# Performance work log

Measured on AMD Instinct MI355X. Metric: run time of the kernel, lower is better.

Reference implementation:

```python
import jax, jax.numpy as jnp
import numpy as np

B = 64          # batch
N = 256         # input_dim (number of MPS sites / pixels)
BOND = 128      # bond dimension
DF = 2          # feature dimension per pixel
OUT = 10        # output classes
EPS = 1e-12


def _xavier_uniform(key, shape, fan_in, fan_out, gain):
    bound = gain * np.sqrt(6.0 / (fan_in + fan_out))
    return jax.random.uniform(key, shape, jnp.float32, -bound, bound)


def setup_inputs() -> dict:
    key = jax.random.key(0)
    k_x, k_c0, k_cr, k_cl = jax.random.split(key, 4)
    gain = float(np.sqrt(2.0 / (1.0 + 0.01 ** 2)))  # leaky_relu gain
    x = jax.random.uniform(k_x, (B, N), dtype=jnp.float32)  # pixels in [0,1]
    # core 0: (1, DF, BOND); torch fan_in = DF*BOND, fan_out = 1*BOND
    core0 = _xavier_uniform(k_c0, (1, DF, BOND), DF * BOND, BOND, gain)
    # remaining N-1 cores: (BOND, DF, BOND); fan_in = DF*BOND, fan_out = BOND*BOND... torch: fan_in = shape[1]*shape[2] = DF*BOND, fan_out = shape[0]*shape[2] = BOND*BOND? No: fan_out = shape[0]*prod(shape[2:]) = BOND*BOND
    cores = _xavier_uniform(k_cr, (N - 1, BOND, DF, BOND), DF * BOND, BOND * BOND, gain)
    classifier = _xavier_uniform(k_cl, (OUT, BOND), BOND, OUT, gain)
    return {"x": x, "core0": core0, "cores": cores, "classifier": classifier}


def _mps_forward(x, core0, cores, classifier):
    b = x.shape[0]
    H = core0.shape[-1]
    # feature map: pixel v -> (1-v, v)
    feats = jnp.stack([1.0 - x, x], axis=-1)                  # (B, N, DF)
    # contract each core with its pixel feature
    special = jnp.einsum('ldh,bd->blh', core0, feats[:, 0])   # (B, 1, H)
    others = jnp.einsum('nldh,bnd->bnlh', cores, feats[:, 1:])  # (B, N-1, H, H)
    log_norm = jnp.zeros((b,), dtype=x.dtype)

    # log-depth tree contraction; loop bound is static (trace-time)
    while 1 + others.shape[1] > 1:
        # pad the special (1,H) leftmost tensor up to (H,H) with zero rows
        padded = jnp.pad(special, ((0, 0), (0, H - special.shape[1]), (0, 0)))
        full = jnp.concatenate([padded[:, None], others], axis=1)  # (B, K, H, H)
        K = full.shape[1]
        odd = (K % 2 != 0)
        if odd:
            last = full[:, -1]
            full = full[:, :-1]
        s1 = full[:, 0::2]                                    # (B, P, H, H)
        s2 = full[:, 1::2]
        cp = jnp.matmul(s1, s2)                               # (B, P, H, H)
        norms = jnp.maximum(
            jnp.sqrt(jnp.sum(cp * cp, axis=(-2, -1))), EPS)   # (B, P)
        log_norm = log_norm + jnp.sum(jnp.log(norms), axis=1)
        cp = cp / norms[:, :, None, None]
        special = cp[:, 0, 0:1, :]                            # keep only row 0
        others = cp[:, 1:]
        if odd:
            others = jnp.concatenate([others, last[:, None]], axis=1)

    mps_out = special[:, 0, :]                                # (B, H)
    logits = mps_out @ classifier.T + log_norm[:, None]      # (B, OUT)
    return logits


def reference(x, core0, cores, classifier):
    return _mps_forward(x, core0, cores, classifier)
```

## Files before the change

### kernel.cpp

```cpp
#include <hip/hip_runtime.h>
#include <stdint.h>


typedef unsigned short u16;
typedef __attribute__((ext_vector_type(8))) short short8;
typedef __attribute__((ext_vector_type(4))) float f32x4;

#define HP 136

__device__ __forceinline__ u16 f2b(float f) {
  uint32_t u = __builtin_bit_cast(uint32_t, f);
  u += 0x7FFFu + ((u >> 16) & 1u);
  return (u16)(u >> 16);
}
__device__ __forceinline__ float b2f(u16 b) {
  uint32_t u = ((uint32_t)b) << 16;
  return __builtin_bit_cast(float, u);
}

struct AccW { f32x4 t[2][2]; };

__device__ __forceinline__ void mfma_w16(const u16* Alds, const u16* Blds,
                                         AccW& acc) {
  const int tid = threadIdx.x;
  const int wid = tid >> 6, lane = tid & 63;
  const int wm = (wid >> 2) * 32, wn = (wid & 3) * 32;
  const int l16 = lane & 15, quad = lane >> 4;
#pragma unroll
  for (int tm = 0; tm < 2; tm++)
#pragma unroll
    for (int tn = 0; tn < 2; tn++)
      acc.t[tm][tn] = (f32x4){0.f, 0.f, 0.f, 0.f};
#pragma unroll
  for (int kk = 0; kk < 128; kk += 32) {
    short8 af[2], bf[2];
#pragma unroll
    for (int t = 0; t < 2; t++) {
      af[t] = *(const short8*)(Alds + (wm + t * 16 + l16) * HP + kk + quad * 8);
      bf[t] = *(const short8*)(Blds + (wn + t * 16 + l16) * HP + kk + quad * 8);
    }
#pragma unroll
    for (int tm = 0; tm < 2; tm++)
#pragma unroll
      for (int tn = 0; tn < 2; tn++)
        acc.t[tm][tn] = __builtin_amdgcn_mfma_f32_16x16x32_bf16(
            af[tm], bf[tn], acc.t[tm][tn], 0, 0, 0);
  }
}

__device__ __forceinline__ float acc_sumsq(const AccW& acc) {
  float ss = 0.f;
#pragma unroll
  for (int tm = 0; tm < 2; tm++)
#pragma unroll
    for (int tn = 0; tn < 2; tn++)
#pragma unroll
      for (int i = 0; i < 4; i++) {
        float v = acc.t[tm][tn][i];
        ss += v * v;
      }
  return ss;
}

__device__ __forceinline__ void bounce_store(u16* Lb, const AccW& acc, float scale,
                                             bool transposed) {
  const int tid = threadIdx.x;
  const int wid = tid >> 6, lane = tid & 63;
  const int wm = (wid >> 2) * 32, wn = (wid & 3) * 32;
  const int l16 = lane & 15, quad = lane >> 4;
#pragma unroll
  for (int tm = 0; tm < 2; tm++)
#pragma unroll
    for (int tn = 0; tn < 2; tn++)
#pragma unroll
      for (int i = 0; i < 4; i++) {
        int r = wm + tm * 16 + quad * 4 + i;
        int c = wn + tn * 16 + l16;
        int key = transposed ? c : r, sec = transposed ? r : c;
        Lb[key * HP + sec] = f2b(acc.t[tm][tn][i] * scale);
      }
}

__device__ __forceinline__ void copy_out(const u16* Lb, u16* out) {
  const int tid = threadIdx.x;
#pragma unroll
  for (int i = 0; i < 2; i++) {
    int g8 = tid + i * 1024;
    int row = g8 >> 4, c8 = g8 & 15;
    *(uint4*)(out + g8 * 8) = *(const uint4*)(Lb + row * HP + c8 * 8);
  }
}

__device__ __forceinline__ void loadM(u16* Lb, const u16* __restrict__ src) {
  const int tid = threadIdx.x;
#pragma unroll
  for (int i = 0; i < 2; i++) {
    int g8 = tid + i * 1024;
    int r = g8 >> 4, c8 = g8 & 15;
    *(uint4*)(Lb + r * HP + c8 * 8) = *(const uint4*)(src + g8 * 8);
  }
}

__device__ __forceinline__ float block_sum(float v, float* red, int nw) {
#pragma unroll
  for (int off = 32; off > 0; off >>= 1) v += __shfl_down(v, off);
  int wid = threadIdx.x >> 6;
  if ((threadIdx.x & 63) == 0) red[wid] = v;
  __syncthreads();
  if (threadIdx.x == 0) {
    float s = 0.f;
    for (int w = 0; w < nw; w++) s += red[w];
    red[0] = s;
  }
  __syncthreads();
  float s = red[0];
  __syncthreads();
  return s;
}

__device__ __forceinline__ float bsum16(float v, float* red) {
#pragma unroll
  for (int off = 32; off > 0; off >>= 1) v += __shfl_down(v, off);
  if ((threadIdx.x & 63) == 0) red[threadIdx.x >> 6] = v;
  __syncthreads();
  float s = 0.f;
#pragma unroll
  for (int w = 0; w < 16; w++) s += red[w];
  return s;
}

__global__ __launch_bounds__(1024) void k1(const float* __restrict__ cores,
                                           u16* __restrict__ T) {
  __shared__ u16 Ald[128 * HP], B0[128 * HP], B1[128 * HP];
  const int j = blockIdx.x;
  const int p = blockIdx.y;
  const float* c1 = cores + (size_t)(2 * j + 1) * 32768;
  const float* c2 = cores + (size_t)(2 * j + 2) * 32768;
  const int tid = threadIdx.x;
#pragma unroll 4
  for (int i = 0; i < 16; i++) {
    int lh = tid + i * 1024;
    int l = lh >> 7, h = lh & 127;
    float a0 = c1[(l * 2 + 0) * 128 + h];
    float av = p ? (c1[(l * 2 + 1) * 128 + h] - a0) : a0;
    Ald[l * HP + h] = f2b(av);
    float b0 = c2[(l * 2 + 0) * 128 + h];
    float b1 = c2[(l * 2 + 1) * 128 + h];
    B0[h * HP + l] = f2b(b0);
    B1[h * HP + l] = f2b(b1 - b0);
  }
  __syncthreads();
  const bool tr = (j % 2) == 0;
  u16* Tj = T + ((size_t)j * 4 + p * 2) * 16384;
  AccW q0, q1;
  mfma_w16(Ald, B0, q0);
  mfma_w16(Ald, B1, q1);
  __syncthreads();
  bounce_store(Ald, q0, 1.f, tr); __syncthreads();
  copy_out(Ald, Tj + 0 * 16384);  __syncthreads();
  bounce_store(Ald, q1, 1.f, tr); __syncthreads();
  copy_out(Ald, Tj + 1 * 16384);
}

__global__ __launch_bounds__(1024, 8) void k1b(const u16* __restrict__ T,
                                               u16* __restrict__ TT) {
  __shared__ u16 Ald[128 * HP], Bld[128 * HP];
  const int t = blockIdx.x;
  const int j2 = blockIdx.y;
  const int m1 = 2 * j2 + 1, m2 = 2 * j2 + 2;
  const u16* TA = T + ((size_t)m1 * 4 + (t >> 2)) * 16384;
  const u16* TB = T + ((size_t)m2 * 4 + (t & 3)) * 16384;
  loadM(Ald, TA);
  loadM(Bld, TB);
  __syncthreads();
  AccW acc;
  mfma_w16(Ald, Bld, acc);
  __syncthreads();
  bounce_store(Ald, acc, 1.f, (j2 % 2) == 0);
  __syncthreads();
  copy_out(Ald, TT + ((size_t)j2 * 16 + t) * 16384);
}

__global__ __launch_bounds__(256) void k1c(const u16* __restrict__ TT,
                                           float* __restrict__ Gpart) {
  __shared__ float Gp[1024];
  const int j2 = blockIdx.x, kc = blockIdx.y;
  const int tid = threadIdx.x;
  const int w = tid >> 6, lane = tid & 63;
  const int l16 = lane & 15, quad = lane >> 4;
  const u16* V = TT + (size_t)j2 * 16 * 16384 + (size_t)l16 * 16384;
  const int k0 = kc * 4096 + w * 1024;
  f32x4 acc = (f32x4){0.f, 0.f, 0.f, 0.f};
  for (int kk = k0; kk < k0 + 1024; kk += 32) {
    short8 av = *(const short8*)(V + kk + quad * 8);
    acc = __builtin_amdgcn_mfma_f32_16x16x32_bf16(av, av, acc, 0, 0, 0);
  }
#pragma unroll
  for (int i = 0; i < 4; i++)
    Gp[w * 256 + (quad * 4 + i) * 16 + l16] = acc[i];
  __syncthreads();
  Gpart[((size_t)j2 * 4 + kc) * 256 + tid] =
      Gp[tid] + Gp[256 + tid] + Gp[512 + tid] + Gp[768 + tid];
}

__global__ __launch_bounds__(128) void k2ns(const float* __restrict__ x,
                                            const float* __restrict__ Gpart,
                                            const float* __restrict__ core0,
                                            const float* __restrict__ cores,
                                            const u16* __restrict__ T,
                                            float* __restrict__ cbuf,
                                            float* __restrict__ sA,
                                            float* __restrict__ logs) {
  __shared__ float Gs[256];
  __shared__ float svec[128];
  __shared__ float red[8];
  const int bx = blockIdx.x, tid = threadIdx.x;
  if (bx < 63) {
    const int j2 = bx;
#pragma unroll
    for (int i = 0; i < 2; i++) {
      int t2 = tid + i * 128;
      float s = 0.f;
#pragma unroll
      for (int kc = 0; kc < 4; kc++)
        s += Gpart[((size_t)j2 * 4 + kc) * 256 + t2];
      Gs[t2] = s;
    }
    __syncthreads();
    if (tid < 64) {
      const int b = tid;
      const float* xb = x + b * 256;
      const int m1 = 2 * j2 + 1, m2 = 2 * j2 + 2;
      float a1 = xb[2 * m1 + 2], b1 = xb[2 * m1 + 3];
      float a2 = xb[2 * m2 + 2], b2 = xb[2 * m2 + 3];
      float c1[4] = {1.f, b1, a1, a1 * b1};
      float c2[4] = {1.f, b2, a2, a2 * b2};
      float c[16];
#pragma unroll
      for (int p = 0; p < 4; p++)
#pragma unroll
        for (int q = 0; q < 4; q++) c[p * 4 + q] = c1[p] * c2[q];
      float n2 = 0.f;
#pragma unroll
      for (int t = 0; t < 16; t++) {
        float s = 0.f;
#pragma unroll
        for (int u = 0; u < 16; u++) s += Gs[t * 16 + u] * c[u];
        n2 += c[t] * s;
      }
      float n = fmaxf(sqrtf(n2), 1e-12f);
      logs[b * 127 + 1 + j2] = logf(n);
      float inv = 1.f / n;
#pragma unroll
      for (int t = 0; t < 16; t++)
        cbuf[((size_t)j2 * 64 + b) * 16 + t] = c[t] * inv;
    }
  } else {
    const int b = bx - 63;
    const float* xb = x + b * 256;
    float x0 = xb[0], x1 = xb[1];
    svec[tid] = core0[tid] * (1.f - x0) + core0[128 + tid] * x0;
    __syncthreads();
    float acc1 = 0.f;
    for (int k = 0; k < 128; k++) {
      float m0 = cores[(k * 2 + 0) * 128 + tid];
      float m1 = cores[(k * 2 + 1) * 128 + tid];
      acc1 += svec[k] * (m0 + x1 * (m1 - m0));
    }
    float tot = block_sum(acc1 * acc1, red, 2);
    float n1 = fmaxf(sqrtf(tot), 1e-12f);
    float ln = logf(n1);
    svec[tid] = acc1 / n1;
    __syncthreads();
    float a = xb[2], bb = xb[3], ab = a * bb;
    float acc2 = 0.f;
    for (int k8 = 0; k8 < 16; k8++) {
      union { uint4 v; u16 s[8]; } q00, q01, q10, q11;
      q00.v = *(const uint4*)(T + tid * 128 + k8 * 8);
      q01.v = *(const uint4*)(T + 16384 + tid * 128 + k8 * 8);
      q10.v = *(const uint4*)(T + 32768 + tid * 128 + k8 * 8);
      q11.v = *(const uint4*)(T + 49152 + tid * 128 + k8 * 8);
#pragma unroll
      for (int e = 0; e < 8; e++) {
        float pk = b2f(q00.s[e]) + a * b2f(q10.s[e]) + bb * b2f(q01.s[e]) +
                   ab * b2f(q11.s[e]);
        acc2 += svec[k8 * 8 + e] * pk;
      }
    }
    float tot2 = block_sum(acc2 * acc2, red, 2);
    float n2 = fmaxf(sqrtf(tot2), 1e-12f);
    sA[b * 128 + tid] = acc2 / n2;
    if (tid == 0) logs[b * 127 + 0] = ln + logf(n2);
  }
}

__global__ __launch_bounds__(256, 4) void k2c(const u16* __restrict__ TT,
                                              const float* __restrict__ cbuf,
                                              u16* __restrict__ M0) {
  const int slice = blockIdx.x;
  const int j2 = blockIdx.y;
  const int tid = threadIdx.x;
  const int e0 = slice * 1024 + tid * 4;
  float v[16][4];
#pragma unroll
  for (int t = 0; t < 16; t++) {
    union { uint2 u; u16 s[4]; } q;
    q.u = *(const uint2*)(TT + ((size_t)j2 * 16 + t) * 16384 + e0);
#pragma unroll
    for (int e = 0; e < 4; e++) v[t][e] = b2f(q.s[e]);
  }
  const float4* cb4 = (const float4*)(cbuf + (size_t)j2 * 1024);
  u16* out = M0 + (size_t)j2 * 16384 + e0;
#pragma unroll 4
  for (int b = 0; b < 64; b++) {
    float4 c0 = cb4[b * 4 + 0];
    float4 c1 = cb4[b * 4 + 1];
    float4 c2 = cb4[b * 4 + 2];
    float4 c3 = cb4[b * 4 + 3];
    float cc[16] = {c0.x, c0.y, c0.z, c0.w, c1.x, c1.y, c1.z, c1.w,
                    c2.x, c2.y, c2.z, c2.w, c3.x, c3.y, c3.z, c3.w};
    float o[4] = {0.f, 0.f, 0.f, 0.f};
#pragma unroll
    for (int t = 0; t < 16; t++)
#pragma unroll
      for (int e = 0; e < 4; e++) o[e] += cc[t] * v[t][e];
    union { uint2 u; u16 s[4]; } r;
#pragma unroll
    for (int e = 0; e < 4; e++) r.s[e] = f2b(o[e]);
    *(uint2*)(out + (size_t)b * 63 * 16384) = r.u;
  }
}

__global__ __launch_bounds__(1024, 4) void round2x(const u16* __restrict__ In,
                                                   u16* __restrict__ Out,
                                                   const float* __restrict__ sIn,
                                                   float* __restrict__ sOut,
                                                   float* __restrict__ logs,
                                                   int count_in, int count_out,
                                                   int slot0, int slot1) {
  __shared__ u16 L0[128 * HP], L1[128 * HP];
  __shared__ float svf[256];
  __shared__ float red[16];
  const int b = blockIdx.y, p = blockIdx.x, tid = threadIdx.x;
  const u16* base = In + (size_t)b * count_in * 16384;
  if (p == 0) {
    if (tid < 128) svf[tid] = sIn[b * 128 + tid];
    loadM(L0, base + 1 * 16384);
    loadM(L1, base + 2 * 16384);
    __syncthreads();
    float acc0 = 0.f;
    if (tid < 128) {
      for (int k8 = 0; k8 < 16; k8++) {
        union { uint4 v; u16 s[8]; } q;
        q.v = *(const uint4*)(base + tid * 128 + k8 * 8);
#pragma unroll
        for (int e = 0; e < 8; e++) acc0 += svf[k8 * 8 + e] * b2f(q.s[e]);
      }
    }
    AccW accq;
    mfma_w16(L0, L1, accq);
    __syncthreads();
    bounce_store(L0, accq, 1.f, true);
    if (tid < 128) svf[128 + tid] = acc0;
    if (tid == 0) {
      logs[b * 127 + slot0] = 0.f;
      logs[b * 127 + slot0 + 1] = 0.f;
    }
    __syncthreads();
    float acc2 = 0.f;
    if (tid < 128) {
      for (int l = 0; l < 128; l++) acc2 += svf[128 + l] * b2f(L0[tid * HP + l]);
    }
    float t2 = bsum16((tid < 128) ? acc2 * acc2 : 0.f, red);
    float n2 = fmaxf(sqrtf(t2), 1e-12f);
    if (tid == 0) logs[b * 127 + slot1] = logf(n2);
    if (tid < 128) sOut[b * 128 + tid] = acc2 / n2;
  } else {
    const int m = p - 1;
    loadM(L0, base + (size_t)(4 * m + 3) * 16384);
    loadM(L1, base + (size_t)(4 * m + 4) * 16384);
    __syncthreads();
    AccW a1;
    mfma_w16(L0, L1, a1);
    __syncthreads();
    loadM(L0, base + (size_t)(4 * m + 5) * 16384);
    loadM(L1, base + (size_t)(4 * m + 6) * 16384);
    __syncthreads();
    AccW a2;
    mfma_w16(L0, L1, a2);
    __syncthreads();
    bounce_store(L0, a1, 1.f, false);
    bounce_store(L1, a2, 1.f, true);
    if (tid == 0) {
      logs[b * 127 + slot0 + 2 + 2 * m] = 0.f;
      logs[b * 127 + slot0 + 3 + 2 * m] = 0.f;
    }
    __syncthreads();
    AccW a3;
    mfma_w16(L0, L1, a3);
    float t3 = bsum16(acc_sumsq(a3), red);
    float n3 = fmaxf(sqrtf(t3), 1e-12f);
    if (tid == 0) logs[b * 127 + slot1 + 1 + m] = logf(n3);
    bounce_store(L0, a3, 1.f / n3, (m % 2) == 0);
    __syncthreads();
    copy_out(L0, Out + ((size_t)b * count_out + m) * 16384);
  }
}

__global__ __launch_bounds__(1024, 8) void r7f(const u16* __restrict__ In,
                                               const float* __restrict__ sIn,
                                               const float* __restrict__ logs,
                                               const float* __restrict__ cls,
                                               float* __restrict__ out) {
  __shared__ u16 Ald[128 * HP], Bld[128 * HP];
  __shared__ float svec[128], ovec[128], red[16];
  const int b = blockIdx.x, tid = threadIdx.x;
  if (tid < 128) svec[tid] = sIn[b * 128 + tid];
  loadM(Ald, In + ((size_t)b * 3 + 1) * 16384);
  loadM(Bld, In + ((size_t)b * 3 + 2) * 16384);
  __syncthreads();
  AccW acc;
  mfma_w16(Ald, Bld, acc);
  const u16* M0p = In + (size_t)b * 3 * 16384;
  float acc0 = 0.f;
  if (tid < 128) {
    for (int k8 = 0; k8 < 16; k8++) {
      union { uint4 v; u16 s[8]; } q;
      q.v = *(const uint4*)(M0p + tid * 128 + k8 * 8);
#pragma unroll
      for (int e = 0; e < 8; e++) acc0 += svec[k8 * 8 + e] * b2f(q.s[e]);
    }
  }
  __syncthreads();
  bounce_store(Ald, acc, 1.f, true);
  if (tid < 128) ovec[tid] = acc0;
  __syncthreads();
  float acc2 = 0.f;
  if (tid < 128) {
    for (int r = 0; r < 128; r++) acc2 += ovec[r] * b2f(Ald[tid * HP + r]);
  }
  float tot = bsum16((tid < 128) ? acc2 * acc2 : 0.f, red);
  float n = fmaxf(sqrtf(tot), 1e-12f);
  float lg = logf(n);
  if (tid < 128) svec[tid] = acc2 / n;
  __syncthreads();
  if (tid < 10) {
    float a = 0.f;
    for (int h = 0; h < 128; h++) a += svec[h] * cls[tid * 128 + h];
    float L = lg;
    for (int i = 0; i < 124; i++) L += logs[b * 127 + i];
    out[b * 10 + tid] = a + L;
  }
}

extern "C" void kernel_launch(void* const* d_in, const int* in_sizes, int n_in,
                              void* d_out, int out_size, void* d_ws, size_t ws_size,
                              hipStream_t stream) {
  (void)in_sizes; (void)n_in; (void)out_size; (void)ws_size;
  const float* x     = (const float*)d_in[0];
  const float* core0 = (const float*)d_in[1];
  const float* cores = (const float*)d_in[2];
  const float* cls   = (const float*)d_in[3];
  float* out = (float*)d_out;
  char* ws = (char*)d_ws;

  constexpr size_t SZ_T  = (size_t)127 * 4 * 16384 * 2;
  constexpr size_t SZ_A  = (size_t)64 * 31 * 16384 * 2;
  constexpr size_t SZ_M0 = (size_t)64 * 63 * 16384 * 2;

  u16*   T    = (u16*)(ws);
  u16*   TT   = (u16*)(ws + SZ_T);
  u16*   M2   = (u16*)(ws);
  u16*   M0   = (u16*)(ws + SZ_A);
  char*  tail0 = ws + SZ_A + SZ_M0;
  float* Gpart = (float*)(tail0);
  float* cbuf = (float*)(tail0 + 262144);
  float* sA   = (float*)(tail0 + 262144 + 262144);
  float* sB   = (float*)(tail0 + 262144 + 262144 + 32768);
  float* logs = (float*)(tail0 + 262144 + 262144 + 65536);

  k1  <<<dim3(127, 2), 1024, 0, stream>>>(cores, T);
  k1b <<<dim3(16, 63), 1024, 0, stream>>>(T, TT);
  k1c <<<dim3(63, 4), 256, 0, stream>>>(TT, Gpart);
  k2ns<<<dim3(127), 128, 0, stream>>>(x, Gpart, core0, cores, T, cbuf, sA, logs);
  k2c <<<dim3(16, 63), 256, 0, stream>>>(TT, cbuf, M0);
  round2x<<<dim3(16, 64), 1024, 0, stream>>>(M0, M2, sA, sB, logs, 63, 15, 64, 96);
  round2x<<<dim3(4, 64), 1024, 0, stream>>>(M2, M0, sB, sA, logs, 15, 3, 112, 120);
  r7f  <<<dim3(64), 1024, 0, stream>>>(M0, sA, logs, cls, out);
}
```

Measured before the change: 247.3 us.

## Replace precomputed 16-term pair products with per-batch fused matmul in k2f

```diff
diff --git a/kernel.cpp b/kernel.cpp
--- a/kernel.cpp
+++ b/kernel.cpp
@@ -162,173 +162,109 @@
   copy_out(Ald, Tj + 1 * 16384);
 }
 
-__global__ __launch_bounds__(1024, 8) void k1b(const u16* __restrict__ T,
-                                               u16* __restrict__ TT) {
-  __shared__ u16 Ald[128 * HP], Bld[128 * HP];
-  const int t = blockIdx.x;
-  const int j2 = blockIdx.y;
-  const int m1 = 2 * j2 + 1, m2 = 2 * j2 + 2;
-  const u16* TA = T + ((size_t)m1 * 4 + (t >> 2)) * 16384;
-  const u16* TB = T + ((size_t)m2 * 4 + (t & 3)) * 16384;
-  loadM(Ald, TA);
-  loadM(Bld, TB);
-  __syncthreads();
-  AccW acc;
-  mfma_w16(Ald, Bld, acc);
-  __syncthreads();
-  bounce_store(Ald, acc, 1.f, (j2 % 2) == 0);
-  __syncthreads();
-  copy_out(Ald, TT + ((size_t)j2 * 16 + t) * 16384);
-}
-
-__global__ __launch_bounds__(256) void k1c(const u16* __restrict__ TT,
-                                           float* __restrict__ Gpart) {
-  __shared__ float Gp[1024];
-  const int j2 = blockIdx.x, kc = blockIdx.y;
-  const int tid = threadIdx.x;
-  const int w = tid >> 6, lane = tid & 63;
-  const int l16 = lane & 15, quad = lane >> 4;
-  const u16* V = TT + (size_t)j2 * 16 * 16384 + (size_t)l16 * 16384;
-  const int k0 = kc * 4096 + w * 1024;
-  f32x4 acc = (f32x4){0.f, 0.f, 0.f, 0.f};
-  for (int kk = k0; kk < k0 + 1024; kk += 32) {
-    short8 av = *(const short8*)(V + kk + quad * 8);
-    acc = __builtin_amdgcn_mfma_f32_16x16x32_bf16(av, av, acc, 0, 0, 0);
-  }
-#pragma unroll
-  for (int i = 0; i < 4; i++)
-    Gp[w * 256 + (quad * 4 + i) * 16 + l16] = acc[i];
-  __syncthreads();
-  Gpart[((size_t)j2 * 4 + kc) * 256 + tid] =
-      Gp[tid] + Gp[256 + tid] + Gp[512 + tid] + Gp[768 + tid];
+__global__ __launch_bounds__(1024, 4) void k2f(const u16* __restrict__ T,
+                                               const float* __restrict__ x,
+                                               u16* __restrict__ M0,
+                                               float* __restrict__ logs) {
+  __shared__ u16 L0[128 * HP], L1[128 * HP];
+  __shared__ float red[16];
+  const int j2 = blockIdx.x, g = blockIdx.y, tid = threadIdx.x;
+  const u16* TA = T + ((size_t)(2 * j2 + 1) * 4) * 16384;
+  const u16* TB = T + ((size_t)(2 * j2 + 2) * 4) * 16384;
+  uint4 rA[2][4], rB[2][4];
+#pragma unroll
+  for (int i = 0; i < 2; i++) {
+    int gg = (tid + i * 1024) * 8;
+#pragma unroll
+    for (int p = 0; p < 4; p++) {
+      rA[i][p] = *(const uint4*)(TA + (size_t)p * 16384 + gg);
+      rB[i][p] = *(const uint4*)(TB + (size_t)p * 16384 + gg);
+    }
+  }
+  for (int bb = 0; bb < 8; bb++) {
+    const int b = g * 8 + bb;
+    const float* xb = x + b * 256;
+    float a1 = xb[4 * j2 + 4], b1 = xb[4 * j2 + 5];
+    float a2 = xb[4 * j2 + 6], b2 = xb[4 * j2 + 7];
+    float ab1 = a1 * b1, ab2 = a2 * b2;
+#pragma unroll
+    for (int i = 0; i < 2; i++) {
+      int gg = tid + i * 1024;
+      int row = gg >> 4, c8 = gg & 15;
+      union { uint4 v; u16 s[8]; } q0, q1, q2, q3, oA, oB;
+      q0.v = rA[i][0]; q1.v = rA[i][1]; q2.v = rA[i][2]; q3.v = rA[i][3];
+#pragma unroll
+      for (int e = 0; e < 8; e++) {
+        float v = b2f(q0.s[e]) + b1 * b2f(q1.s[e]) + a1 * b2f(q2.s[e]) +
+                  ab1 * b2f(q3.s[e]);
+        oA.s[e] = f2b(v);
+      }
+      q0.v = rB[i][0]; q1.v = rB[i][1]; q2.v = rB[i][2]; q3.v = rB[i][3];
+#pragma unroll
+      for (int e = 0; e < 8; e++) {
+        float v = b2f(q0.s[e]) + b2 * b2f(q1.s[e]) + a2 * b2f(q2.s[e]) +
+                  ab2 * b2f(q3.s[e]);
+        oB.s[e] = f2b(v);
+      }
+      *(uint4*)(L0 + row * HP + c8 * 8) = oA.v;
+      *(uint4*)(L1 + row * HP + c8 * 8) = oB.v;
+    }
+    __syncthreads();
+    AccW acc;
+    mfma_w16(L0, L1, acc);
+    float t = bsum16(acc_sumsq(acc), red);
+    float n = fmaxf(sqrtf(t), 1e-12f);
+    if (tid == 0) logs[b * 127 + 1 + j2] = logf(n);
+    bounce_store(L0, acc, 1.f / n, (j2 % 2) == 0);
+    __syncthreads();
+    copy_out(L0, M0 + ((size_t)b * 63 + j2) * 16384);
+    __syncthreads();
+  }
 }
 
 __global__ __launch_bounds__(128) void k2ns(const float* __restrict__ x,
-                                            const float* __restrict__ Gpart,
                                             const float* __restrict__ core0,
                                             const float* __restrict__ cores,
                                             const u16* __restrict__ T,
-                                            float* __restrict__ cbuf,
                                             float* __restrict__ sA,
                                             float* __restrict__ logs) {
-  __shared__ float Gs[256];
   __shared__ float svec[128];
   __shared__ float red[8];
-  const int bx = blockIdx.x, tid = threadIdx.x;
-  if (bx < 63) {
-    const int j2 = bx;
-#pragma unroll
-    for (int i = 0; i < 2; i++) {
-      int t2 = tid + i * 128;
-      float s = 0.f;
-#pragma unroll
-      for (int kc = 0; kc < 4; kc++)
-        s += Gpart[((size_t)j2 * 4 + kc) * 256 + t2];
-      Gs[t2] = s;
-    }
-    __syncthreads();
-    if (tid < 64) {
-      const int b = tid;
-      const float* xb = x + b * 256;
-      const int m1 = 2 * j2 + 1, m2 = 2 * j2 + 2;
-      float a1 = xb[2 * m1 + 2], b1 = xb[2 * m1 + 3];
-      float a2 = xb[2 * m2 + 2], b2 = xb[2 * m2 + 3];
-      float c1[4] = {1.f, b1, a1, a1 * b1};
-      float c2[4] = {1.f, b2, a2, a2 * b2};
-      float c[16];
-#pragma unroll
-      for (int p = 0; p < 4; p++)
-#pragma unroll
-        for (int q = 0; q < 4; q++) c[p * 4 + q] = c1[p] * c2[q];
-      float n2 = 0.f;
-#pragma unroll
-      for (int t = 0; t < 16; t++) {
-        float s = 0.f;
-#pragma unroll
-        for (int u = 0; u < 16; u++) s += Gs[t * 16 + u] * c[u];
-        n2 += c[t] * s;
-      }
-      float n = fmaxf(sqrtf(n2), 1e-12f);
-      logs[b * 127 + 1 + j2] = logf(n);
-      float inv = 1.f / n;
-#pragma unroll
-      for (int t = 0; t < 16; t++)
-        cbuf[((size_t)j2 * 64 + b) * 16 + t] = c[t] * inv;
-    }
-  } else {
-    const int b = bx - 63;
-    const float* xb = x + b * 256;
-    float x0 = xb[0], x1 = xb[1];
-    svec[tid] = core0[tid] * (1.f - x0) + core0[128 + tid] * x0;
-    __syncthreads();
-    float acc1 = 0.f;
-    for (int k = 0; k < 128; k++) {
-      float m0 = cores[(k * 2 + 0) * 128 + tid];
-      float m1 = cores[(k * 2 + 1) * 128 + tid];
-      acc1 += svec[k] * (m0 + x1 * (m1 - m0));
-    }
-    float tot = block_sum(acc1 * acc1, red, 2);
-    float n1 = fmaxf(sqrtf(tot), 1e-12f);
-    float ln = logf(n1);
-    svec[tid] = acc1 / n1;
-    __syncthreads();
-    float a = xb[2], bb = xb[3], ab = a * bb;
-    float acc2 = 0.f;
-    for (int k8 = 0; k8 < 16; k8++) {
-      union { uint4 v; u16 s[8]; } q00, q01, q10, q11;
-      q00.v = *(const uint4*)(T + tid * 128 + k8 * 8);
-      q01.v = *(const uint4*)(T + 16384 + tid * 128 + k8 * 8);
-      q10.v = *(const uint4*)(T + 32768 + tid * 128 + k8 * 8);
-      q11.v = *(const uint4*)(T + 49152 + tid * 128 + k8 * 8);
-#pragma unroll
-      for (int e = 0; e < 8; e++) {
-        float pk = b2f(q00.s[e]) + a * b2f(q10.s[e]) + bb * b2f(q01.s[e]) +
-                   ab * b2f(q11.s[e]);
-        acc2 += svec[k8 * 8 + e] * pk;
-      }
-    }
-    float tot2 = block_sum(acc2 * acc2, red, 2);
-    float n2 = fmaxf(sqrtf(tot2), 1e-12f);
-    sA[b * 128 + tid] = acc2 / n2;
-    if (tid == 0) logs[b * 127 + 0] = ln + logf(n2);
-  }
-}
-
-__global__ __launch_bounds__(256, 4) void k2c(const u16* __restrict__ TT,
-                                              const float* __restrict__ cbuf,
-                                              u16* __restrict__ M0) {
-  const int slice = blockIdx.x;
-  const int j2 = blockIdx.y;
-  const int tid = threadIdx.x;
-  const int e0 = slice * 1024 + tid * 4;
-  float v[16][4];
-#pragma unroll
-  for (int t = 0; t < 16; t++) {
-    union { uint2 u; u16 s[4]; } q;
-    q.u = *(const uint2*)(TT + ((size_t)j2 * 16 + t) * 16384 + e0);
-#pragma unroll
-    for (int e = 0; e < 4; e++) v[t][e] = b2f(q.s[e]);
-  }
-  const float4* cb4 = (const float4*)(cbuf + (size_t)j2 * 1024);
-  u16* out = M0 + (size_t)j2 * 16384 + e0;
-#pragma unroll 4
-  for (int b = 0; b < 64; b++) {
-    float4 c0 = cb4[b * 4 + 0];
-    float4 c1 = cb4[b * 4 + 1];
-    float4 c2 = cb4[b * 4 + 2];
-    float4 c3 = cb4[b * 4 + 3];
-    float cc[16] = {c0.x, c0.y, c0.z, c0.w, c1.x, c1.y, c1.z, c1.w,
-                    c2.x, c2.y, c2.z, c2.w, c3.x, c3.y, c3.z, c3.w};
-    float o[4] = {0.f, 0.f, 0.f, 0.f};
-#pragma unroll
-    for (int t = 0; t < 16; t++)
-#pragma unroll
-      for (int e = 0; e < 4; e++) o[e] += cc[t] * v[t][e];
-    union { uint2 u; u16 s[4]; } r;
-#pragma unroll
-    for (int e = 0; e < 4; e++) r.s[e] = f2b(o[e]);
-    *(uint2*)(out + (size_t)b * 63 * 16384) = r.u;
-  }
+  const int b = blockIdx.x, tid = threadIdx.x;
+  const float* xb = x + b * 256;
+  float x0 = xb[0], x1 = xb[1];
+  svec[tid] = core0[tid] * (1.f - x0) + core0[128 + tid] * x0;
+  __syncthreads();
+  float acc1 = 0.f;
+  for (int k = 0; k < 128; k++) {
+    float m0 = cores[(k * 2 + 0) * 128 + tid];
+    float m1 = cores[(k * 2 + 1) * 128 + tid];
+    acc1 += svec[k] * (m0 + x1 * (m1 - m0));
+  }
+  float tot = block_sum(acc1 * acc1, red, 2);
+  float n1 = fmaxf(sqrtf(tot), 1e-12f);
+  float ln = logf(n1);
+  svec[tid] = acc1 / n1;
+  __syncthreads();
+  float a = xb[2], bb = xb[3], ab = a * bb;
+  float acc2 = 0.f;
+  for (int k8 = 0; k8 < 16; k8++) {
+    union { uint4 v; u16 s[8]; } q00, q01, q10, q11;
+    q00.v = *(const uint4*)(T + tid * 128 + k8 * 8);
+    q01.v = *(const uint4*)(T + 16384 + tid * 128 + k8 * 8);
+    q10.v = *(const uint4*)(T + 32768 + tid * 128 + k8 * 8);
+    q11.v = *(const uint4*)(T + 49152 + tid * 128 + k8 * 8);
+#pragma unroll
+    for (int e = 0; e < 8; e++) {
+      float pk = b2f(q00.s[e]) + a * b2f(q10.s[e]) + bb * b2f(q01.s[e]) +
+                 ab * b2f(q11.s[e]);
+      acc2 += svec[k8 * 8 + e] * pk;
+    }
+  }
+  float tot2 = block_sum(acc2 * acc2, red, 2);
+  float n2 = fmaxf(sqrtf(tot2), 1e-12f);
+  sA[b * 128 + tid] = acc2 / n2;
+  if (tid == 0) logs[b * 127 + 0] = ln + logf(n2);
 }
 
 __global__ __launch_bounds__(1024, 4) void round2x(const u16* __restrict__ In,
@@ -464,26 +400,20 @@
   float* out = (float*)d_out;
   char* ws = (char*)d_ws;
 
-  constexpr size_t SZ_T  = (size_t)127 * 4 * 16384 * 2;
   constexpr size_t SZ_A  = (size_t)64 * 31 * 16384 * 2;
   constexpr size_t SZ_M0 = (size_t)64 * 63 * 16384 * 2;
 
   u16*   T    = (u16*)(ws);
-  u16*   TT   = (u16*)(ws + SZ_T);
   u16*   M2   = (u16*)(ws);
   u16*   M0   = (u16*)(ws + SZ_A);
   char*  tail0 = ws + SZ_A + SZ_M0;
-  float* Gpart = (float*)(tail0);
-  float* cbuf = (float*)(tail0 + 262144);
   float* sA   = (float*)(tail0 + 262144 + 262144);
   float* sB   = (float*)(tail0 + 262144 + 262144 + 32768);
   float* logs = (float*)(tail0 + 262144 + 262144 + 65536);
 
   k1  <<<dim3(127, 2), 1024, 0, stream>>>(cores, T);
-  k1b <<<dim3(16, 63), 1024, 0, stream>>>(T, TT);
-  k1c <<<dim3(63, 4), 256, 0, stream>>>(TT, Gpart);
-  k2ns<<<dim3(127), 128, 0, stream>>>(x, Gpart, core0, cores, T, cbuf, sA, logs);
-  k2c <<<dim3(16, 63), 256, 0, stream>>>(TT, cbuf, M0);
+  k2f <<<dim3(63, 8), 1024, 0, stream>>>(T, x, M0, logs);
+  k2ns<<<dim3(64), 128, 0, stream>>>(x, core0, cores, T, sA, logs);
   round2x<<<dim3(16, 64), 1024, 0, stream>>>(M0, M2, sA, sB, logs, 63, 15, 64, 96);
   round2x<<<dim3(4, 64), 1024, 0, stream>>>(M2, M0, sB, sA, logs, 15, 3, 112, 120);
   r7f  <<<dim3(64), 1024, 0, stream>>>(M0, sA, logs, cls, out);
```

Result: slower. 464.4 us (+87.8%).
